# Performance work log

Hardware: AMD Instinct MI355X
Metric: run time of the kernel (lower is better)

The kernel has to match this reference:

```python
import jax, jax.numpy as jnp
import numpy as np
import math

B, N, M, C, H = 4, 2048, 2048, 512, 4
D_V = C // H          # 128, used for scale and value head dim
D_QK = 2 * C // H     # 256, q/k head dim due to seq-axis split of the 2*dim qkv output
SCALE = D_V ** -0.5
EPS = 1e-12           # F.normalize eps


def _l2norm(t):
    n = jnp.linalg.norm(t, axis=-1, keepdims=True)
    return t / jnp.maximum(n, EPS)


def setup_inputs() -> dict:
    key = jax.random.key(0)
    k1, k2, k3, k4 = jax.random.split(key, 4)
    x = jax.random.normal(k1, (B, N, C), dtype=jnp.float32)
    context = jax.random.normal(k2, (B, M, C), dtype=jnp.float32)
    W_qkv = jax.random.normal(k3, (2 * C, C), dtype=jnp.float32) * 0.02  # torch Linear weight [out,in]
    W_proj = jax.random.normal(k4, (C, C), dtype=jnp.float32) * 0.02
    radius = jnp.ones((H,), dtype=jnp.float32) * math.sqrt(D_V)
    return {"x": x, "context": context, "W_qkv": W_qkv, "W_proj": W_proj, "radius": radius}


def reference(x, context, W_qkv, W_proj, radius):
    # qkv(cat([x, context], dim=1)) then split along sequence: q from x rows, k from context rows
    q = jnp.einsum('bnc,oc->bno', x, W_qkv)        # [B,N,2C]
    k = jnp.einsum('bmc,oc->bmo', context, W_qkv)  # [B,M,2C]
    q = q.reshape(B, N, H, D_QK).transpose(0, 2, 1, 3)       # [B,H,N,256]
    k = k.reshape(B, M, H, D_QK).transpose(0, 2, 1, 3)       # [B,H,M,256]
    v = context.reshape(B, M, H, D_V).transpose(0, 2, 1, 3)  # [B,H,M,128]
    r = radius[None, :, None, None]
    q = _l2norm(q) * r
    k = _l2norm(k) * r
    attn = jnp.einsum('bhnd,bhmd->bhnm', q, k) * SCALE
    attn = jax.nn.softmax(attn, axis=-1)
    out = jnp.einsum('bhnm,bhmd->bhnd', attn, v)
    out = out.transpose(0, 2, 1, 3).reshape(B, N, C)
    return jnp.einsum('bnc,oc->bno', out, W_proj)
```

## Files before the change

kernel.cpp:

```cpp
#include <hip/hip_runtime.h>
#include <hip/hip_bf16.h>
#include <stdint.h>

#define SCALE_F 0.08838834764831845f

typedef __attribute__((ext_vector_type(8))) short short8;
typedef __attribute__((ext_vector_type(4))) float f32x4;
typedef __attribute__((ext_vector_type(16))) float f32x16;

__device__ __forceinline__ void g2l16(const void* g, void* l) {
  __builtin_amdgcn_global_load_lds(
      (const __attribute__((address_space(1))) void*)g,
      (__attribute__((address_space(3))) void*)l, 16, 0, 0);
}

__global__ __launch_bounds__(256) void convert_all(
    const float* __restrict__ x, const float* __restrict__ ctx,
    const float* __restrict__ wqkv, const float* __restrict__ wproj,
    __hip_bfloat16* __restrict__ ab, __hip_bfloat16* __restrict__ wb,
    __hip_bfloat16* __restrict__ wpb)
{
  size_t qi = (size_t)blockIdx.x * 256 + threadIdx.x;
  const float* src; __hip_bfloat16* dst; size_t off;
  if (qi < 1048576)      { src = x;     dst = ab;           off = qi; }
  else if (qi < 2097152) { src = ctx;   dst = ab + 4194304; off = qi - 1048576; }
  else if (qi < 2228224) { src = wqkv;  dst = wb;           off = qi - 2097152; }
  else                   { src = wproj; dst = wpb;          off = qi - 2228224; }
  float4 v = ((const float4*)src)[off];
  union { __hip_bfloat16 h4[4]; uint2 u; } o;
  o.h4[0] = __float2bfloat16(v.x); o.h4[1] = __float2bfloat16(v.y);
  o.h4[2] = __float2bfloat16(v.z); o.h4[3] = __float2bfloat16(v.w);
  ((uint2*)dst)[off] = o.u;
}

__global__ __launch_bounds__(256) void transpose_v(
    const float* __restrict__ ctx, __hip_bfloat16* __restrict__ vt)
{
  __shared__ float tile[128][33];
  const int bid = blockIdx.x;
  const int mt = bid & 63;
  const int bh = bid >> 6;
  const int h = bh & 3, b = bh >> 2;
  const int tid = threadIdx.x;
  for (int i = 0; i < 16; ++i) {
    int idx = i * 256 + tid;
    int mm = idx >> 7, d = idx & 127;
    tile[d][mm] = ctx[((size_t)b * 2048 + mt * 32 + mm) * 512 + h * 128 + d];
  }
  __syncthreads();
  for (int i = 0; i < 16; ++i) {
    int idx = i * 256 + tid;
    int d = idx >> 5, mm = idx & 31;
    vt[((size_t)bh * 128 + d) * 2048 + mt * 32 + mm] = __float2bfloat16(tile[d][mm]);
  }
}

__global__ __launch_bounds__(256) void gemm_nt(
    const __hip_bfloat16* __restrict__ A, const __hip_bfloat16* __restrict__ B,
    float* __restrict__ C, int O, int K, int tiles_o)
{
  __shared__ __hip_bfloat16 sA[128 * 32];
  __shared__ __hip_bfloat16 sB[128 * 32];
  const int tid = threadIdx.x;
  const int wave = tid >> 6, lane = tid & 63;
  const int ln = lane & 15, q = lane >> 4;
  const int br = (blockIdx.x / tiles_o) * 128;
  const int bo = (blockIdx.x % tiles_o) * 128;
  const int wr = (wave >> 1) * 64, wc = (wave & 1) * 64;
  const __hip_bfloat16* Ab = A + (size_t)br * K;
  const __hip_bfloat16* Bb = B + (size_t)bo * K;
  const int row0 = tid >> 2, p0 = tid & 3;
  f32x4 acc[4][4] = {};
  for (int k0 = 0; k0 < K; k0 += 32) {
    for (int i = 0; i < 2; ++i) {
      int row = i * 64 + row0;
      g2l16(Ab + (size_t)row * K + k0 + p0 * 8, (char*)sA + (i * 256 + tid) * 16);
      g2l16(Bb + (size_t)row * K + k0 + p0 * 8, (char*)sB + (i * 256 + tid) * 16);
    }
    __syncthreads();
    short8 af[4], bfr[4];
    for (int mi = 0; mi < 4; ++mi)
      af[mi] = *(const short8*)(sA + (wr + mi * 16 + ln) * 32 + q * 8);
    for (int ni = 0; ni < 4; ++ni)
      bfr[ni] = *(const short8*)(sB + (wc + ni * 16 + ln) * 32 + q * 8);
    for (int mi = 0; mi < 4; ++mi)
      for (int ni = 0; ni < 4; ++ni)
        acc[mi][ni] = __builtin_amdgcn_mfma_f32_16x16x32_bf16(af[mi], bfr[ni], acc[mi][ni], 0, 0, 0);
    __syncthreads();
  }
  for (int mi = 0; mi < 4; ++mi)
    for (int ni = 0; ni < 4; ++ni) {
      int rg = br + wr + mi * 16 + q * 4;
      int cg = bo + wc + ni * 16 + ln;
      for (int r = 0; r < 4; ++r)
        C[(size_t)(rg + r) * O + cg] = acc[mi][ni][r];
    }
}

__global__ __launch_bounds__(256) void normalize_qk(
    const float* __restrict__ proj, const float* __restrict__ radius,
    __hip_bfloat16* __restrict__ qn, __hip_bfloat16* __restrict__ kn)
{
  const int r = blockIdx.x;
  const int h = threadIdx.x >> 6, lane = threadIdx.x & 63;
  float4 v = *(const float4*)(proj + (size_t)r * 1024 + h * 256 + lane * 4);
  float ss = v.x * v.x + v.y * v.y + v.z * v.z + v.w * v.w;
  for (int off = 1; off < 64; off <<= 1) ss += __shfl_xor(ss, off);
  float nrm = fmaxf(sqrtf(ss), 1e-12f);
  const bool isq = r < 8192;
  const int rr = isq ? r : r - 8192;
  const float rad = radius[h];
  const float sc = (isq ? rad * rad * SCALE_F : 1.0f) / nrm;
  __hip_bfloat16* dst = (isq ? qn : kn) +
      ((size_t)((rr >> 11) * 4 + h) * 2048 + (rr & 2047)) * 256 + lane * 4;
  union { __hip_bfloat16 h4[4]; uint2 u; } o;
  o.h4[0] = __float2bfloat16(v.x * sc);
  o.h4[1] = __float2bfloat16(v.y * sc);
  o.h4[2] = __float2bfloat16(v.z * sc);
  o.h4[3] = __float2bfloat16(v.w * sc);
  *(uint2*)dst = o.u;
}

__global__ __launch_bounds__(256, 1) void attn(
    const __hip_bfloat16* __restrict__ qn,
    const __hip_bfloat16* __restrict__ kn,
    const __hip_bfloat16* __restrict__ vt,
    __hip_bfloat16* __restrict__ ob)
{
  __shared__ __hip_bfloat16 sK[2][32 * 256];
  __shared__ __hip_bfloat16 sV[2][128 * 32];
  __shared__ __hip_bfloat16 sP[4][32 * 40];
  const int tid = threadIdx.x, wave = tid >> 6, lane = tid & 63;
  const int m32 = lane & 31, hi = lane >> 5;
  const int nt = blockIdx.x & 15, bh = blockIdx.x >> 4;
  const __hip_bfloat16* Q = qn + ((size_t)bh * 2048 + nt * 128 + wave * 32) * 256;
  const __hip_bfloat16* Kp = kn + (size_t)bh * 2048 * 256;
  const __hip_bfloat16* Vp = vt + (size_t)bh * 128 * 2048;

  short8 qf[16];
  for (int kk = 0; kk < 16; ++kk)
    qf[kk] = *(const short8*)(Q + m32 * 256 + kk * 16 + hi * 8);

  f32x16 oacc[4];
  float denom[16];
  for (int i = 0; i < 4; ++i)
    for (int j = 0; j < 16; ++j) oacc[i][j] = 0.f;
  for (int j = 0; j < 16; ++j) denom[j] = 0.f;
  __hip_bfloat16* sPw = sP[wave];

  for (int i = 0; i < 4; ++i) {
    int D = i * 256 + tid, row = D >> 5, cc = D & 31;
    g2l16(Kp + (size_t)row * 256 + ((cc ^ (row & 7)) << 3), (char*)sK[0] + D * 16);
  }
  for (int i = 0; i < 2; ++i) {
    int D = i * 256 + tid, rd = D >> 2, cc = D & 3;
    g2l16(Vp + (size_t)rd * 2048 + ((cc ^ ((rd >> 1) & 3)) << 3), (char*)sV[0] + D * 16);
  }
  __syncthreads();

  for (int it = 0; it < 64; ++it) {
    const int cur = it & 1, nxt = cur ^ 1;
    if (it + 1 < 64) {
      const int m1 = (it + 1) * 32;
      for (int i = 0; i < 4; ++i) {
        int D = i * 256 + tid, row = D >> 5, cc = D & 31;
        g2l16(Kp + (size_t)(m1 + row) * 256 + ((cc ^ (row & 7)) << 3),
              (char*)sK[nxt] + D * 16);
      }
      for (int i = 0; i < 2; ++i) {
        int D = i * 256 + tid, rd = D >> 2, cc = D & 3;
        g2l16(Vp + (size_t)rd * 2048 + m1 + ((cc ^ ((rd >> 1) & 3)) << 3),
              (char*)sV[nxt] + D * 16);
      }
    }
    const __hip_bfloat16* sKc = sK[cur];
    f32x16 s;
    for (int j = 0; j < 16; ++j) s[j] = 0.f;
    for (int kk = 0; kk < 16; ++kk) {
      int c = kk * 2 + hi;
      short8 kf = *(const short8*)(sKc + m32 * 256 + ((c ^ (m32 & 7)) << 3));
      s = __builtin_amdgcn_mfma_f32_32x32x16_bf16(qf[kk], kf, s, 0, 0, 0);
    }
    for (int reg = 0; reg < 16; ++reg) {
      float e = __expf(s[reg]);
      denom[reg] += e;
      int row = (reg & 3) + 8 * (reg >> 2) + 4 * hi;
      sPw[row * 40 + m32] = __float2bfloat16(e);
    }
    asm volatile("s_waitcnt lgkmcnt(0)" ::: "memory");
    const __hip_bfloat16* sVc = sV[cur];
    for (int kc = 0; kc < 2; ++kc) {
      short8 pf = *(const short8*)(sPw + m32 * 40 + kc * 16 + hi * 8);
      for (int vi = 0; vi < 4; ++vi) {
        int rd = vi * 32 + m32;
        int c = kc * 2 + hi;
        short8 vf = *(const short8*)(sVc + rd * 32 + ((c ^ ((rd >> 1) & 3)) << 3));
        oacc[vi] = __builtin_amdgcn_mfma_f32_32x32x16_bf16(pf, vf, oacc[vi], 0, 0, 0);
      }
    }
    __syncthreads();
  }

  for (int reg = 0; reg < 16; ++reg)
    for (int off = 1; off < 32; off <<= 1)
      denom[reg] += __shfl_xor(denom[reg], off);

  const int b = bh >> 2, h = bh & 3;
  for (int vi = 0; vi < 4; ++vi)
    for (int reg = 0; reg < 16; ++reg) {
      int row = nt * 128 + wave * 32 + (reg & 3) + 8 * (reg >> 2) + 4 * hi;
      float o = oacc[vi][reg] / denom[reg];
      ob[((size_t)b * 2048 + row) * 512 + h * 128 + vi * 32 + m32] = __float2bfloat16(o);
    }
}

extern "C" void kernel_launch(void* const* d_in, const int* in_sizes, int n_in,
                              void* d_out, int out_size, void* d_ws, size_t ws_size,
                              hipStream_t stream) {
  const float* x      = (const float*)d_in[0];
  const float* ctx    = (const float*)d_in[1];
  const float* wqkv   = (const float*)d_in[2];
  const float* wproj  = (const float*)d_in[3];
  const float* radius = (const float*)d_in[4];
  char* ws = (char*)d_ws;
  __hip_bfloat16* ab  = (__hip_bfloat16*)(ws);
  __hip_bfloat16* wb  = (__hip_bfloat16*)(ws + 16777216);
  __hip_bfloat16* wpb = (__hip_bfloat16*)(ws + 17825792);
  float*          proj= (float*)(ws + 18350080);
  __hip_bfloat16* qn  = (__hip_bfloat16*)(ws + 85458944);
  __hip_bfloat16* kn  = (__hip_bfloat16*)(ws + 102236160);
  __hip_bfloat16* vt  = (__hip_bfloat16*)(ws + 119013376);
  __hip_bfloat16* ob  = (__hip_bfloat16*)(ws + 127401984);
  float* out = (float*)d_out;

  convert_all<<<8960, 256, 0, stream>>>(x, ctx, wqkv, wproj, ab, wb, wpb);
  transpose_v<<<1024, 256, 0, stream>>>(ctx, vt);
  gemm_nt<<<1024, 256, 0, stream>>>(ab, wb, proj, 1024, 512, 8);
  normalize_qk<<<16384, 256, 0, stream>>>(proj, radius, qn, kn);
  attn<<<256, 256, 0, stream>>>(qn, kn, vt, ob);
  gemm_nt<<<256, 256, 0, stream>>>(ob, wpb, out, 512, 512, 4);
}
```

Baseline: 253.3 us.

## Split attention over key halves with fp32 partials and a combine kernel

The attention kernel now splits the 2048 context keys into two halves, launching 512 blocks instead of 256 so that more work is available across CUs. It also allows two blocks per CU. Each half writes unnormalized fp32 partial outputs and row denominators into the reused proj workspace. A new combine kernel sums the two halves, divides by the total denominator and writes bf16. The QK^T loop is also split into two independent MFMA accumulation chains to improve instruction-level parallelism. The cost is extra global traffic for the fp32 partials, one more kernel launch, and more register pressure under the tighter launch bound.

```diff
diff --git a/kernel.cpp b/kernel.cpp
--- a/kernel.cpp
+++ b/kernel.cpp
@@ -121,18 +121,23 @@
   *(uint2*)dst = o.u;
 }
 
-__global__ __launch_bounds__(256, 1) void attn(
+__global__ __launch_bounds__(256, 2) void attn(
     const __hip_bfloat16* __restrict__ qn,
     const __hip_bfloat16* __restrict__ kn,
     const __hip_bfloat16* __restrict__ vt,
-    __hip_bfloat16* __restrict__ ob)
+    float* __restrict__ Op,
+    float* __restrict__ den)
 {
   __shared__ __hip_bfloat16 sK[2][32 * 256];
   __shared__ __hip_bfloat16 sV[2][128 * 32];
   __shared__ __hip_bfloat16 sP[4][32 * 40];
   const int tid = threadIdx.x, wave = tid >> 6, lane = tid & 63;
   const int m32 = lane & 31, hi = lane >> 5;
-  const int nt = blockIdx.x & 15, bh = blockIdx.x >> 4;
+  const int i = blockIdx.x;
+  const int bh = (i & 7) + 8 * ((i >> 3) & 1);
+  const int half = (i >> 4) & 1;
+  const int nt = i >> 5;
+  const int mbase = half * 1024;
   const __hip_bfloat16* Q = qn + ((size_t)bh * 2048 + nt * 128 + wave * 32) * 256;
   const __hip_bfloat16* Kp = kn + (size_t)bh * 2048 * 256;
   const __hip_bfloat16* Vp = vt + (size_t)bh * 128 * 2048;
@@ -143,46 +148,50 @@
 
   f32x16 oacc[4];
   float denom[16];
-  for (int i = 0; i < 4; ++i)
-    for (int j = 0; j < 16; ++j) oacc[i][j] = 0.f;
+  for (int v = 0; v < 4; ++v)
+    for (int j = 0; j < 16; ++j) oacc[v][j] = 0.f;
   for (int j = 0; j < 16; ++j) denom[j] = 0.f;
   __hip_bfloat16* sPw = sP[wave];
 
-  for (int i = 0; i < 4; ++i) {
-    int D = i * 256 + tid, row = D >> 5, cc = D & 31;
-    g2l16(Kp + (size_t)row * 256 + ((cc ^ (row & 7)) << 3), (char*)sK[0] + D * 16);
-  }
-  for (int i = 0; i < 2; ++i) {
-    int D = i * 256 + tid, rd = D >> 2, cc = D & 3;
-    g2l16(Vp + (size_t)rd * 2048 + ((cc ^ ((rd >> 1) & 3)) << 3), (char*)sV[0] + D * 16);
+  for (int t = 0; t < 4; ++t) {
+    int D = t * 256 + tid, row = D >> 5, cc = D & 31;
+    g2l16(Kp + (size_t)(mbase + row) * 256 + ((cc ^ (row & 7)) << 3),
+          (char*)sK[0] + D * 16);
+  }
+  for (int t = 0; t < 2; ++t) {
+    int D = t * 256 + tid, rd = D >> 2, cc = D & 3;
+    g2l16(Vp + (size_t)rd * 2048 + mbase + ((cc ^ ((rd >> 1) & 3)) << 3),
+          (char*)sV[0] + D * 16);
   }
   __syncthreads();
 
-  for (int it = 0; it < 64; ++it) {
+  for (int it = 0; it < 32; ++it) {
     const int cur = it & 1, nxt = cur ^ 1;
-    if (it + 1 < 64) {
-      const int m1 = (it + 1) * 32;
-      for (int i = 0; i < 4; ++i) {
-        int D = i * 256 + tid, row = D >> 5, cc = D & 31;
+    if (it + 1 < 32) {
+      const int m1 = mbase + (it + 1) * 32;
+      for (int t = 0; t < 4; ++t) {
+        int D = t * 256 + tid, row = D >> 5, cc = D & 31;
         g2l16(Kp + (size_t)(m1 + row) * 256 + ((cc ^ (row & 7)) << 3),
               (char*)sK[nxt] + D * 16);
       }
-      for (int i = 0; i < 2; ++i) {
-        int D = i * 256 + tid, rd = D >> 2, cc = D & 3;
+      for (int t = 0; t < 2; ++t) {
+        int D = t * 256 + tid, rd = D >> 2, cc = D & 3;
         g2l16(Vp + (size_t)rd * 2048 + m1 + ((cc ^ ((rd >> 1) & 3)) << 3),
               (char*)sV[nxt] + D * 16);
       }
     }
     const __hip_bfloat16* sKc = sK[cur];
-    f32x16 s;
-    for (int j = 0; j < 16; ++j) s[j] = 0.f;
-    for (int kk = 0; kk < 16; ++kk) {
-      int c = kk * 2 + hi;
-      short8 kf = *(const short8*)(sKc + m32 * 256 + ((c ^ (m32 & 7)) << 3));
-      s = __builtin_amdgcn_mfma_f32_32x32x16_bf16(qf[kk], kf, s, 0, 0, 0);
+    f32x16 sa, sb;
+    for (int j = 0; j < 16; ++j) { sa[j] = 0.f; sb[j] = 0.f; }
+    for (int kk = 0; kk < 8; ++kk) {
+      int ca = kk * 2 + hi, cb = (kk + 8) * 2 + hi;
+      short8 kfa = *(const short8*)(sKc + m32 * 256 + ((ca ^ (m32 & 7)) << 3));
+      short8 kfb = *(const short8*)(sKc + m32 * 256 + ((cb ^ (m32 & 7)) << 3));
+      sa = __builtin_amdgcn_mfma_f32_32x32x16_bf16(qf[kk], kfa, sa, 0, 0, 0);
+      sb = __builtin_amdgcn_mfma_f32_32x32x16_bf16(qf[kk + 8], kfb, sb, 0, 0, 0);
     }
     for (int reg = 0; reg < 16; ++reg) {
-      float e = __expf(s[reg]);
+      float e = __expf(sa[reg] + sb[reg]);
       denom[reg] += e;
       int row = (reg & 3) + 8 * (reg >> 2) + 4 * hi;
       sPw[row * 40 + m32] = __float2bfloat16(e);
@@ -205,13 +214,36 @@
     for (int off = 1; off < 32; off <<= 1)
       denom[reg] += __shfl_xor(denom[reg], off);
 
-  const int b = bh >> 2, h = bh & 3;
+  float* Opb = Op + ((size_t)(half * 16 + bh) * 2048) * 128;
+  float* denb = den + (size_t)(half * 16 + bh) * 2048;
+  const int rbase = nt * 128 + wave * 32;
   for (int vi = 0; vi < 4; ++vi)
     for (int reg = 0; reg < 16; ++reg) {
-      int row = nt * 128 + wave * 32 + (reg & 3) + 8 * (reg >> 2) + 4 * hi;
-      float o = oacc[vi][reg] / denom[reg];
-      ob[((size_t)b * 2048 + row) * 512 + h * 128 + vi * 32 + m32] = __float2bfloat16(o);
-    }
+      int row = rbase + (reg & 3) + 8 * (reg >> 2) + 4 * hi;
+      Opb[(size_t)row * 128 + vi * 32 + m32] = oacc[vi][reg];
+    }
+  if (m32 == 0)
+    for (int reg = 0; reg < 16; ++reg)
+      denb[rbase + (reg & 3) + 8 * (reg >> 2) + 4 * hi] = denom[reg];
+}
+
+__global__ __launch_bounds__(256) void combine(
+    const float* __restrict__ Op, const float* __restrict__ den,
+    __hip_bfloat16* __restrict__ ob)
+{
+  int qi = blockIdx.x * 256 + threadIdx.x;
+  int r = qi >> 5, dq = qi & 5 * 6 + 1;
+  dq = qi & 31;
+  int bh = r >> 11, n = r & 2047, b = bh >> 2, h = bh & 3;
+  float4 o0 = ((const float4*)Op)[qi];
+  float4 o1 = ((const float4*)(Op + 4194304))[qi];
+  float inv = 1.0f / (den[r] + den[32768 + r]);
+  union { __hip_bfloat16 h4[4]; uint2 u; } o;
+  o.h4[0] = __float2bfloat16((o0.x + o1.x) * inv);
+  o.h4[1] = __float2bfloat16((o0.y + o1.y) * inv);
+  o.h4[2] = __float2bfloat16((o0.z + o1.z) * inv);
+  o.h4[3] = __float2bfloat16((o0.w + o1.w) * inv);
+  *(uint2*)&ob[((size_t)b * 2048 + n) * 512 + h * 128 + dq * 4] = o.u;
 }
 
 extern "C" void kernel_launch(void* const* d_in, const int* in_sizes, int n_in,
@@ -227,6 +259,8 @@
   __hip_bfloat16* wb  = (__hip_bfloat16*)(ws + 16777216);
   __hip_bfloat16* wpb = (__hip_bfloat16*)(ws + 17825792);
   float*          proj= (float*)(ws + 18350080);
+  float*          Op  = proj;
+  float*          den = (float*)(ws + 18350080 + 33554432);
   __hip_bfloat16* qn  = (__hip_bfloat16*)(ws + 85458944);
   __hip_bfloat16* kn  = (__hip_bfloat16*)(ws + 102236160);
   __hip_bfloat16* vt  = (__hip_bfloat16*)(ws + 119013376);
@@ -237,6 +271,7 @@
   transpose_v<<<1024, 256, 0, stream>>>(ctx, vt);
   gemm_nt<<<1024, 256, 0, stream>>>(ab, wb, proj, 1024, 512, 8);
   normalize_qk<<<16384, 256, 0, stream>>>(proj, radius, qn, kn);
-  attn<<<256, 256, 0, stream>>>(qn, kn, vt, ob);
+  attn<<<512, 256, 0, stream>>>(qn, kn, vt, Op, den);
+  combine<<<4096, 256, 0, stream>>>(Op, den, ob);
   gemm_nt<<<256, 256, 0, stream>>>(ob, wpb, out, 512, 512, 4);
 }
```

Result: faster. 227.2 us (-10.3%).
